# Kernel optimization log

Measured on AMD Instinct MI355X. Metric: run time of the kernel, lower is better.

The kernel has to match this reference:

```python
import jax, jax.numpy as jnp
import numpy as np

B, N, D, H = 4096, 64, 32, 64

def setup_inputs() -> dict:
    key = jax.random.key(0)
    ks = jax.random.split(key, 10)
    s = lambda fan_in: 1.0 / np.sqrt(fan_in)
    return {
        "joint_features": jax.random.normal(ks[0], (B, N, D), jnp.float32),
        "Wm1": jax.random.uniform(ks[1], (2 * D, H), jnp.float32, -s(2 * D), s(2 * D)),
        "bm1": jax.random.uniform(ks[2], (H,), jnp.float32, -s(2 * D), s(2 * D)),
        "Wm2": jax.random.uniform(ks[3], (H, D), jnp.float32, -s(H), s(H)),
        "bm2": jax.random.uniform(ks[4], (D,), jnp.float32, -s(H), s(H)),
        "Wu1": jax.random.uniform(ks[5], (2 * D, H), jnp.float32, -s(2 * D), s(2 * D)),
        "bu1": jax.random.uniform(ks[6], (H,), jnp.float32, -s(2 * D), s(2 * D)),
        "Wu2": jax.random.uniform(ks[7], (H, D), jnp.float32, -s(H), s(H)),
        "bu2": jax.random.uniform(ks[8], (D,), jnp.float32, -s(H), s(H)),
        "residual_weight": jnp.float32(0.5),
        "num_joints": N,
    }

def reference(joint_features, Wm1, bm1, Wm2, bm2, Wu1, bu1, Wu2, bu2, residual_weight, num_joints):
    n = num_joints
    # chain topology: directed edges (i->i+1) and (i+1->i); dst receives message
    dst = jnp.concatenate([jnp.arange(n - 1), jnp.arange(1, n)])  # [E]
    src = jnp.concatenate([jnp.arange(1, n), jnp.arange(n - 1)])  # [E]
    # edge gather + concat: [B, E, 2D]
    edge_in = jnp.concatenate([joint_features[:, dst], joint_features[:, src]], axis=-1)
    # message MLP (ReLU after both layers, per original Sequential)
    msg = jax.nn.relu(jax.nn.relu(edge_in @ Wm1 + bm1) @ Wm2 + bm2)  # [B, E, D]
    # scatter-add messages to destination nodes
    messages = jnp.zeros_like(joint_features).at[:, dst].add(msg)  # [B, N, D]
    # per-node update MLP on concat(feature, message)
    upd_in = jnp.concatenate([joint_features, messages], axis=-1)  # [B, N, 2D]
    updated = jax.nn.relu(upd_in @ Wu1 + bu1) @ Wu2 + bu2  # [B, N, D]
    return residual_weight * updated + (1.0 - residual_weight) * joint_features
```

## Files before the change

### kernel.cpp

```cpp
#include <hip/hip_runtime.h>
#include <hip/hip_bf16.h>


typedef __bf16 bf16x8 __attribute__((ext_vector_type(8)));
typedef float  f32x4  __attribute__((ext_vector_type(4)));
typedef unsigned short u16;

#define NBATCH 8
#define NBI 2
#define ITERS (NBATCH / NBI)
#define HS  72
#define MBS 40

__device__ __forceinline__ u16 f2b(float f) { return __builtin_bit_cast(u16, (__bf16)f); }
__device__ __forceinline__ f32x4 MFMA(bf16x8 a, bf16x8 b, f32x4 c) {
    return __builtin_amdgcn_mfma_f32_16x16x32_bf16(a, b, c, 0, 0, 0);
}
__device__ __forceinline__ bf16x8 pack8(float4 a, float4 b) {
    bf16x8 r = {(__bf16)a.x, (__bf16)a.y, (__bf16)a.z, (__bf16)a.w,
                (__bf16)b.x, (__bf16)b.y, (__bf16)b.z, (__bf16)b.w};
    return r;
}

__global__ __launch_bounds__(256, 2)
void agn_mfma(const float* __restrict__ x, const float* __restrict__ Wm1,
              const float* __restrict__ bm1, const float* __restrict__ Wm2,
              const float* __restrict__ bm2, const float* __restrict__ Wu1,
              const float* __restrict__ bu1, const float* __restrict__ Wu2,
              const float* __restrict__ bu2, const float* __restrict__ rw_p,
              float* __restrict__ out)
{
    __shared__ __align__(16) u16 sH[256 * HS];
    __shared__ __align__(16) u16 sMB[256 * MBS];

    const int t = threadIdx.x;
    const int w = t >> 6;
    const int lane = t & 63;
    const int ln = lane & 15;
    const int q  = lane >> 4;

    bf16x8 B1a[4], B1b[4], B2[2][2], B3[2][4], B4[2][2];
#pragma unroll
    for (int nt = 0; nt < 4; ++nt)
#pragma unroll
        for (int j = 0; j < 8; ++j) {
            B1a[nt][j] = (__bf16)Wm1[(q * 8 + j) * 64 + nt * 16 + ln];
            B1b[nt][j] = (__bf16)Wm1[(32 + q * 8 + j) * 64 + nt * 16 + ln];
        }
#pragma unroll
    for (int s = 0; s < 2; ++s)
#pragma unroll
        for (int nt = 0; nt < 2; ++nt)
#pragma unroll
            for (int j = 0; j < 8; ++j)
                B2[s][nt][j] = (__bf16)Wm2[(s * 32 + q * 8 + j) * 32 + nt * 16 + ln];
#pragma unroll
    for (int s = 0; s < 2; ++s)
#pragma unroll
        for (int nt = 0; nt < 4; ++nt)
#pragma unroll
            for (int j = 0; j < 8; ++j)
                B3[s][nt][j] = (__bf16)Wu1[(s * 32 + q * 8 + j) * 64 + nt * 16 + ln];
#pragma unroll
    for (int s = 0; s < 2; ++s)
#pragma unroll
        for (int nt = 0; nt < 2; ++nt)
#pragma unroll
            for (int j = 0; j < 8; ++j)
                B4[s][nt][j] = (__bf16)Wu2[(s * 32 + q * 8 + j) * 32 + nt * 16 + ln];

    float bm1v[4], bu1v[4], bm2v[2], bu2v[2];
#pragma unroll
    for (int nt = 0; nt < 4; ++nt) { bm1v[nt] = bm1[nt * 16 + ln]; bu1v[nt] = bu1[nt * 16 + ln]; }
#pragma unroll
    for (int nt = 0; nt < 2; ++nt) { bm2v[nt] = bm2[nt * 16 + ln]; bu2v[nt] = bu2[nt * 16 + ln]; }
    const float rw = rw_p[0];
    const float om = 1.f - rw;

    const size_t base = (size_t)blockIdx.x * (NBATCH * 64 * 32);

    for (int it = 0; it < ITERS; ++it) {
        const float* xit = x + base + (size_t)it * (NBI * 64 * 32);
        float*       oit = out + base + (size_t)it * (NBI * 64 * 32);

        {
            float4 xd[4][2], xsv[4][2];
#pragma unroll
            for (int m = 0; m < 4; ++m) {
                const int mt = 4 * w + m;
                const int erow = mt * 16 + ln;
                const int bb = erow >> 7;
                int e = erow & 127;
                if (e >= 126) e = 0;
                const int dst  = (e < 63) ? e : e - 62;
                const int srcn = (e < 63) ? e + 1 : e - 63;
                const float* pd = xit + ((bb << 6) + dst) * 32 + q * 8;
                const float* ps = xit + ((bb << 6) + srcn) * 32 + q * 8;
                xd[m][0] = *(const float4*)pd;  xd[m][1] = *(const float4*)(pd + 4);
                xsv[m][0] = *(const float4*)ps; xsv[m][1] = *(const float4*)(ps + 4);
            }
#pragma unroll
            for (int m = 0; m < 4; ++m) {
                const int mt = 4 * w + m;
                bf16x8 Ad = pack8(xd[m][0], xd[m][1]);
                bf16x8 As = pack8(xsv[m][0], xsv[m][1]);
#pragma unroll
                for (int nt = 0; nt < 4; ++nt) {
                    f32x4 acc = {0.f, 0.f, 0.f, 0.f};
                    acc = MFMA(Ad, B1a[nt], acc);
                    acc = MFMA(As, B1b[nt], acc);
                    const int rb = mt * 16 + q * 4;
                    const int c  = nt * 16 + ln;
#pragma unroll
                    for (int r = 0; r < 4; ++r)
                        sH[(rb + r) * HS + c] = f2b(fmaxf(acc[r] + bm1v[nt], 0.f));
                }
            }
        }
        __syncthreads();

#pragma unroll
        for (int m = 0; m < 4; ++m) {
            const int mt = 4 * w + m;
            const int row = mt * 16 + ln;
            bf16x8 A0 = __builtin_bit_cast(bf16x8, *(const uint4*)&sH[row * HS + q * 8]);
            bf16x8 A1 = __builtin_bit_cast(bf16x8, *(const uint4*)&sH[row * HS + 32 + q * 8]);
#pragma unroll
            for (int nt = 0; nt < 2; ++nt) {
                f32x4 acc = {0.f, 0.f, 0.f, 0.f};
                acc = MFMA(A0, B2[0][nt], acc);
                acc = MFMA(A1, B2[1][nt], acc);
                const int rb = mt * 16 + q * 4;
                const int c  = nt * 16 + ln;
#pragma unroll
                for (int r = 0; r < 4; ++r)
                    sMB[(rb + r) * MBS + c] = f2b(fmaxf(acc[r] + bm2v[nt], 0.f));
            }
        }
        __syncthreads();

#pragma unroll
        for (int m = 0; m < 2; ++m) {
            const int mt = 2 * w + m;
            const int row = mt * 16 + ln;
            const int bb = row >> 6;
            const int i2 = row & 63;
            const float* p = xit + row * 32 + q * 8;
            float4 a0 = *(const float4*)p;
            float4 a1 = *(const float4*)(p + 4);
            bf16x8 A0 = pack8(a0, a1);
            float mv[8] = {0.f, 0.f, 0.f, 0.f, 0.f, 0.f, 0.f, 0.f};
            if (i2 < 63) {
                uint4 u = *(const uint4*)&sMB[((bb << 7) + i2) * MBS + q * 8];
                const unsigned* pu = (const unsigned*)&u;
#pragma unroll
                for (int h = 0; h < 4; ++h) {
                    mv[2 * h]     += __uint_as_float(pu[h] << 16);
                    mv[2 * h + 1] += __uint_as_float(pu[h] & 0xFFFF0000u);
                }
            }
            if (i2 > 0) {
                uint4 u = *(const uint4*)&sMB[((bb << 7) + 62 + i2) * MBS + q * 8];
                const unsigned* pu = (const unsigned*)&u;
#pragma unroll
                for (int h = 0; h < 4; ++h) {
                    mv[2 * h]     += __uint_as_float(pu[h] << 16);
                    mv[2 * h + 1] += __uint_as_float(pu[h] & 0xFFFF0000u);
                }
            }
            bf16x8 A1;
#pragma unroll
            for (int j = 0; j < 8; ++j) A1[j] = (__bf16)mv[j];
#pragma unroll
            for (int nt = 0; nt < 4; ++nt) {
                f32x4 acc = {0.f, 0.f, 0.f, 0.f};
                acc = MFMA(A0, B3[0][nt], acc);
                acc = MFMA(A1, B3[1][nt], acc);
                const int rb = mt * 16 + q * 4;
                const int c  = nt * 16 + ln;
#pragma unroll
                for (int r = 0; r < 4; ++r)
                    sH[(rb + r) * HS + c] = f2b(fmaxf(acc[r] + bu1v[nt], 0.f));
            }
        }
        __syncthreads();

#pragma unroll
        for (int m = 0; m < 2; ++m) {
            const int mt = 2 * w + m;
            const int arow = mt * 16 + ln;
            bf16x8 A0 = __builtin_bit_cast(bf16x8, *(const uint4*)&sH[arow * HS + q * 8]);
            bf16x8 A1 = __builtin_bit_cast(bf16x8, *(const uint4*)&sH[arow * HS + 32 + q * 8]);
#pragma unroll
            for (int nt = 0; nt < 2; ++nt) {
                f32x4 acc = {0.f, 0.f, 0.f, 0.f};
                acc = MFMA(A0, B4[0][nt], acc);
                acc = MFMA(A1, B4[1][nt], acc);
                const int rb = mt * 16 + q * 4;
                const int c  = nt * 16 + ln;
#pragma unroll
                for (int r = 0; r < 4; ++r) {
                    const int off = (rb + r) * 32 + c;
                    oit[off] = rw * (acc[r] + bu2v[nt]) + om * xit[off];
                }
            }
        }
        __syncthreads();
    }
}

extern "C" void kernel_launch(void* const* d_in, const int* in_sizes, int n_in,
                              void* d_out, int out_size, void* d_ws, size_t ws_size,
                              hipStream_t stream) {
    const float* x   = (const float*)d_in[0];
    const float* Wm1 = (const float*)d_in[1];
    const float* bm1 = (const float*)d_in[2];
    const float* Wm2 = (const float*)d_in[3];
    const float* bm2 = (const float*)d_in[4];
    const float* Wu1 = (const float*)d_in[5];
    const float* bu1 = (const float*)d_in[6];
    const float* Wu2 = (const float*)d_in[7];
    const float* bu2 = (const float*)d_in[8];
    const float* rw  = (const float*)d_in[9];
    float* out = (float*)d_out;

    const int B = in_sizes[0] / (64 * 32);
    agn_mfma<<<B / NBATCH, 256, 0, stream>>>(x, Wm1, bm1, Wm2, bm2, Wu1, bu1, Wu2, bu2, rw, out);
}
```

Before: 121.7 us.

## Pre-pack bf16 weight fragments in prep kernel and launch one block per batch

Adds a small prep kernel that converts the weights into bf16 MFMA fragment layout in workspace, along with biases and the residual weight. The main kernel then loads each fragment with a single 16-byte read instead of many scalar converted loads. The main kernel now handles one batch element per block (4096 blocks) with half the LDS and occupancy hint 4, replacing 512 blocks that each looped over 8 batches. Weight fragments are loaded per phase to reduce register pressure, at the cost of an extra kernel launch and re-reading weights in every block.

```diff
diff --git a/kernel.cpp b/kernel.cpp
--- a/kernel.cpp
+++ b/kernel.cpp
@@ -6,9 +6,6 @@
 typedef float  f32x4  __attribute__((ext_vector_type(4)));
 typedef unsigned short u16;
 
-#define NBATCH 8
-#define NBI 2
-#define ITERS (NBATCH / NBI)
 #define HS  72
 #define MBS 40
 
@@ -22,16 +19,47 @@
     return r;
 }
 
-__global__ __launch_bounds__(256, 2)
-void agn_mfma(const float* __restrict__ x, const float* __restrict__ Wm1,
-              const float* __restrict__ bm1, const float* __restrict__ Wm2,
-              const float* __restrict__ bm2, const float* __restrict__ Wu1,
-              const float* __restrict__ bu1, const float* __restrict__ Wu2,
-              const float* __restrict__ bu2, const float* __restrict__ rw_p,
-              float* __restrict__ out)
+__global__ void agn_prep(const float* __restrict__ Wm1, const float* __restrict__ bm1,
+                         const float* __restrict__ Wm2, const float* __restrict__ bm2,
+                         const float* __restrict__ Wu1, const float* __restrict__ bu1,
+                         const float* __restrict__ Wu2, const float* __restrict__ bu2,
+                         const float* __restrict__ rw,
+                         u16* __restrict__ wsf, float* __restrict__ wsb)
 {
-    __shared__ __align__(16) u16 sH[256 * HS];
-    __shared__ __align__(16) u16 sMB[256 * MBS];
+    const int idx = blockIdx.x * 256 + threadIdx.x;
+    {
+        const int f = idx >> 9, r = idx & 511;
+        const int lane = r >> 3, j = r & 7;
+        const int ln = lane & 15, q = lane >> 4;
+        float v;
+        if (f < 4)       v = Wm1[(q * 8 + j) * 64 + f * 16 + ln];
+        else if (f < 8)  v = Wm1[(32 + q * 8 + j) * 64 + (f - 4) * 16 + ln];
+        else if (f < 12) { int s = (f - 8) >> 1, nt = (f - 8) & 1;  v = Wm2[(s * 32 + q * 8 + j) * 32 + nt * 16 + ln]; }
+        else if (f < 20) { int s = (f - 12) >> 2, nt = (f - 12) & 3; v = Wu1[(s * 32 + q * 8 + j) * 64 + nt * 16 + ln]; }
+        else             { int s = (f - 20) >> 1, nt = (f - 20) & 1; v = Wu2[(s * 32 + q * 8 + j) * 32 + nt * 16 + ln]; }
+        wsf[idx] = f2b(v);
+    }
+    if (blockIdx.x == 0) {
+        const int t = threadIdx.x;
+        if (t < 192) {
+            const int g = t >> 4, i = t & 15;
+            float v;
+            if (g < 4)       v = bm1[g * 16 + i];
+            else if (g < 6)  v = bm2[(g - 4) * 16 + i];
+            else if (g < 10) v = bu1[(g - 6) * 16 + i];
+            else             v = bu2[(g - 10) * 16 + i];
+            wsb[t] = v;
+        }
+        if (t == 255) wsb[192] = rw[0];
+    }
+}
+
+__global__ __launch_bounds__(256, 4)
+void agn_main(const float* __restrict__ x, const u16* __restrict__ wsf,
+              const float* __restrict__ wsb, float* __restrict__ out)
+{
+    __shared__ __align__(16) u16 sH[128 * HS];
+    __shared__ __align__(16) u16 sMB[128 * MBS];
 
     const int t = threadIdx.x;
     const int w = t >> 6;
@@ -39,89 +67,58 @@
     const int ln = lane & 15;
     const int q  = lane >> 4;
 
-    bf16x8 B1a[4], B1b[4], B2[2][2], B3[2][4], B4[2][2];
-#pragma unroll
-    for (int nt = 0; nt < 4; ++nt)
-#pragma unroll
-        for (int j = 0; j < 8; ++j) {
-            B1a[nt][j] = (__bf16)Wm1[(q * 8 + j) * 64 + nt * 16 + ln];
-            B1b[nt][j] = (__bf16)Wm1[(32 + q * 8 + j) * 64 + nt * 16 + ln];
-        }
-#pragma unroll
-    for (int s = 0; s < 2; ++s)
-#pragma unroll
-        for (int nt = 0; nt < 2; ++nt)
-#pragma unroll
-            for (int j = 0; j < 8; ++j)
-                B2[s][nt][j] = (__bf16)Wm2[(s * 32 + q * 8 + j) * 32 + nt * 16 + ln];
-#pragma unroll
-    for (int s = 0; s < 2; ++s)
-#pragma unroll
-        for (int nt = 0; nt < 4; ++nt)
-#pragma unroll
-            for (int j = 0; j < 8; ++j)
-                B3[s][nt][j] = (__bf16)Wu1[(s * 32 + q * 8 + j) * 64 + nt * 16 + ln];
-#pragma unroll
-    for (int s = 0; s < 2; ++s)
-#pragma unroll
-        for (int nt = 0; nt < 2; ++nt)
-#pragma unroll
-            for (int j = 0; j < 8; ++j)
-                B4[s][nt][j] = (__bf16)Wu2[(s * 32 + q * 8 + j) * 32 + nt * 16 + ln];
-
-    float bm1v[4], bu1v[4], bm2v[2], bu2v[2];
-#pragma unroll
-    for (int nt = 0; nt < 4; ++nt) { bm1v[nt] = bm1[nt * 16 + ln]; bu1v[nt] = bu1[nt * 16 + ln]; }
-#pragma unroll
-    for (int nt = 0; nt < 2; ++nt) { bm2v[nt] = bm2[nt * 16 + ln]; bu2v[nt] = bu2[nt * 16 + ln]; }
-    const float rw = rw_p[0];
-    const float om = 1.f - rw;
-
-    const size_t base = (size_t)blockIdx.x * (NBATCH * 64 * 32);
-
-    for (int it = 0; it < ITERS; ++it) {
-        const float* xit = x + base + (size_t)it * (NBI * 64 * 32);
-        float*       oit = out + base + (size_t)it * (NBI * 64 * 32);
-
-        {
-            float4 xd[4][2], xsv[4][2];
-#pragma unroll
-            for (int m = 0; m < 4; ++m) {
-                const int mt = 4 * w + m;
-                const int erow = mt * 16 + ln;
-                const int bb = erow >> 7;
-                int e = erow & 127;
-                if (e >= 126) e = 0;
-                const int dst  = (e < 63) ? e : e - 62;
-                const int srcn = (e < 63) ? e + 1 : e - 63;
-                const float* pd = xit + ((bb << 6) + dst) * 32 + q * 8;
-                const float* ps = xit + ((bb << 6) + srcn) * 32 + q * 8;
-                xd[m][0] = *(const float4*)pd;  xd[m][1] = *(const float4*)(pd + 4);
-                xsv[m][0] = *(const float4*)ps; xsv[m][1] = *(const float4*)(ps + 4);
-            }
-#pragma unroll
-            for (int m = 0; m < 4; ++m) {
-                const int mt = 4 * w + m;
-                bf16x8 Ad = pack8(xd[m][0], xd[m][1]);
-                bf16x8 As = pack8(xsv[m][0], xsv[m][1]);
-#pragma unroll
-                for (int nt = 0; nt < 4; ++nt) {
-                    f32x4 acc = {0.f, 0.f, 0.f, 0.f};
-                    acc = MFMA(Ad, B1a[nt], acc);
-                    acc = MFMA(As, B1b[nt], acc);
-                    const int rb = mt * 16 + q * 4;
-                    const int c  = nt * 16 + ln;
-#pragma unroll
-                    for (int r = 0; r < 4; ++r)
-                        sH[(rb + r) * HS + c] = f2b(fmaxf(acc[r] + bm1v[nt], 0.f));
-                }
-            }
-        }
-        __syncthreads();
-
-#pragma unroll
-        for (int m = 0; m < 4; ++m) {
-            const int mt = 4 * w + m;
+    const size_t base = (size_t)blockIdx.x * (64 * 32);
+    const float* xb = x + base;
+    float*       ob = out + base;
+
+    const u16* wf = wsf + lane * 8;
+#define LDFRAG(f) __builtin_bit_cast(bf16x8, *(const uint4*)(wf + ((f) << 9)))
+
+    {
+        bf16x8 B1a[4], B1b[4];
+#pragma unroll
+        for (int nt = 0; nt < 4; ++nt) { B1a[nt] = LDFRAG(nt); B1b[nt] = LDFRAG(4 + nt); }
+        float bm1v[4];
+#pragma unroll
+        for (int nt = 0; nt < 4; ++nt) bm1v[nt] = wsb[nt * 16 + ln];
+#pragma unroll
+        for (int m = 0; m < 2; ++m) {
+            const int mt = 2 * w + m;
+            int e = mt * 16 + ln;
+            if (e >= 126) e = 0;
+            const int dst  = (e < 63) ? e : e - 62;
+            const int srcn = (e < 63) ? e + 1 : e - 63;
+            const float* pd = xb + dst * 32 + q * 8;
+            const float* ps = xb + srcn * 32 + q * 8;
+            float4 d0 = *(const float4*)pd, d1 = *(const float4*)(pd + 4);
+            float4 s0 = *(const float4*)ps, s1 = *(const float4*)(ps + 4);
+            bf16x8 Ad = pack8(d0, d1);
+            bf16x8 As = pack8(s0, s1);
+#pragma unroll
+            for (int nt = 0; nt < 4; ++nt) {
+                f32x4 acc = {0.f, 0.f, 0.f, 0.f};
+                acc = MFMA(Ad, B1a[nt], acc);
+                acc = MFMA(As, B1b[nt], acc);
+                const int rb = mt * 16 + q * 4;
+                const int c  = nt * 16 + ln;
+#pragma unroll
+                for (int r = 0; r < 4; ++r)
+                    sH[(rb + r) * HS + c] = f2b(fmaxf(acc[r] + bm1v[nt], 0.f));
+            }
+        }
+    }
+    __syncthreads();
+
+    {
+        bf16x8 B2[2][2];
+#pragma unroll
+        for (int s = 0; s < 2; ++s)
+#pragma unroll
+            for (int nt = 0; nt < 2; ++nt) B2[s][nt] = LDFRAG(8 + s * 2 + nt);
+        float bm2v[2] = { wsb[64 + ln], wsb[80 + ln] };
+#pragma unroll
+        for (int m = 0; m < 2; ++m) {
+            const int mt = 2 * w + m;
             const int row = mt * 16 + ln;
             bf16x8 A0 = __builtin_bit_cast(bf16x8, *(const uint4*)&sH[row * HS + q * 8]);
             bf16x8 A1 = __builtin_bit_cast(bf16x8, *(const uint4*)&sH[row * HS + 32 + q * 8]);
@@ -137,76 +134,85 @@
                     sMB[(rb + r) * MBS + c] = f2b(fmaxf(acc[r] + bm2v[nt], 0.f));
             }
         }
-        __syncthreads();
-
-#pragma unroll
-        for (int m = 0; m < 2; ++m) {
-            const int mt = 2 * w + m;
-            const int row = mt * 16 + ln;
-            const int bb = row >> 6;
-            const int i2 = row & 63;
-            const float* p = xit + row * 32 + q * 8;
-            float4 a0 = *(const float4*)p;
-            float4 a1 = *(const float4*)(p + 4);
-            bf16x8 A0 = pack8(a0, a1);
-            float mv[8] = {0.f, 0.f, 0.f, 0.f, 0.f, 0.f, 0.f, 0.f};
-            if (i2 < 63) {
-                uint4 u = *(const uint4*)&sMB[((bb << 7) + i2) * MBS + q * 8];
-                const unsigned* pu = (const unsigned*)&u;
-#pragma unroll
-                for (int h = 0; h < 4; ++h) {
-                    mv[2 * h]     += __uint_as_float(pu[h] << 16);
-                    mv[2 * h + 1] += __uint_as_float(pu[h] & 0xFFFF0000u);
-                }
-            }
-            if (i2 > 0) {
-                uint4 u = *(const uint4*)&sMB[((bb << 7) + 62 + i2) * MBS + q * 8];
-                const unsigned* pu = (const unsigned*)&u;
-#pragma unroll
-                for (int h = 0; h < 4; ++h) {
-                    mv[2 * h]     += __uint_as_float(pu[h] << 16);
-                    mv[2 * h + 1] += __uint_as_float(pu[h] & 0xFFFF0000u);
-                }
-            }
-            bf16x8 A1;
-#pragma unroll
-            for (int j = 0; j < 8; ++j) A1[j] = (__bf16)mv[j];
-#pragma unroll
-            for (int nt = 0; nt < 4; ++nt) {
-                f32x4 acc = {0.f, 0.f, 0.f, 0.f};
-                acc = MFMA(A0, B3[0][nt], acc);
-                acc = MFMA(A1, B3[1][nt], acc);
-                const int rb = mt * 16 + q * 4;
-                const int c  = nt * 16 + ln;
-#pragma unroll
-                for (int r = 0; r < 4; ++r)
-                    sH[(rb + r) * HS + c] = f2b(fmaxf(acc[r] + bu1v[nt], 0.f));
-            }
-        }
-        __syncthreads();
-
-#pragma unroll
-        for (int m = 0; m < 2; ++m) {
-            const int mt = 2 * w + m;
-            const int arow = mt * 16 + ln;
-            bf16x8 A0 = __builtin_bit_cast(bf16x8, *(const uint4*)&sH[arow * HS + q * 8]);
-            bf16x8 A1 = __builtin_bit_cast(bf16x8, *(const uint4*)&sH[arow * HS + 32 + q * 8]);
-#pragma unroll
-            for (int nt = 0; nt < 2; ++nt) {
-                f32x4 acc = {0.f, 0.f, 0.f, 0.f};
-                acc = MFMA(A0, B4[0][nt], acc);
-                acc = MFMA(A1, B4[1][nt], acc);
-                const int rb = mt * 16 + q * 4;
-                const int c  = nt * 16 + ln;
-#pragma unroll
-                for (int r = 0; r < 4; ++r) {
-                    const int off = (rb + r) * 32 + c;
-                    oit[off] = rw * (acc[r] + bu2v[nt]) + om * xit[off];
-                }
-            }
-        }
-        __syncthreads();
-    }
+    }
+    __syncthreads();
+
+    {
+        bf16x8 B3[2][4];
+#pragma unroll
+        for (int s = 0; s < 2; ++s)
+#pragma unroll
+            for (int nt = 0; nt < 4; ++nt) B3[s][nt] = LDFRAG(12 + s * 4 + nt);
+        float bu1v[4];
+#pragma unroll
+        for (int nt = 0; nt < 4; ++nt) bu1v[nt] = wsb[96 + nt * 16 + ln];
+        const int row = w * 16 + ln;
+        const float* p = xb + row * 32 + q * 8;
+        float4 a0 = *(const float4*)p, a1 = *(const float4*)(p + 4);
+        bf16x8 A0 = pack8(a0, a1);
+        float mv[8] = {0.f, 0.f, 0.f, 0.f, 0.f, 0.f, 0.f, 0.f};
+        if (row < 63) {
+            uint4 u = *(const uint4*)&sMB[row * MBS + q * 8];
+            const unsigned* pu = (const unsigned*)&u;
+#pragma unroll
+            for (int h = 0; h < 4; ++h) {
+                mv[2 * h]     += __uint_as_float(pu[h] << 16);
+                mv[2 * h + 1] += __uint_as_float(pu[h] & 0xFFFF0000u);
+            }
+        }
+        if (row > 0) {
+            uint4 u = *(const uint4*)&sMB[(62 + row) * MBS + q * 8];
+            const unsigned* pu = (const unsigned*)&u;
+#pragma unroll
+            for (int h = 0; h < 4; ++h) {
+                mv[2 * h]     += __uint_as_float(pu[h] << 16);
+                mv[2 * h + 1] += __uint_as_float(pu[h] & 0xFFFF0000u);
+            }
+        }
+        bf16x8 A1;
+#pragma unroll
+        for (int j = 0; j < 8; ++j) A1[j] = (__bf16)mv[j];
+#pragma unroll
+        for (int nt = 0; nt < 4; ++nt) {
+            f32x4 acc = {0.f, 0.f, 0.f, 0.f};
+            acc = MFMA(A0, B3[0][nt], acc);
+            acc = MFMA(A1, B3[1][nt], acc);
+            const int rb = w * 16 + q * 4;
+            const int c  = nt * 16 + ln;
+#pragma unroll
+            for (int r = 0; r < 4; ++r)
+                sH[(rb + r) * HS + c] = f2b(fmaxf(acc[r] + bu1v[nt], 0.f));
+        }
+    }
+    __syncthreads();
+
+    {
+        bf16x8 B4[2][2];
+#pragma unroll
+        for (int s = 0; s < 2; ++s)
+#pragma unroll
+            for (int nt = 0; nt < 2; ++nt) B4[s][nt] = LDFRAG(20 + s * 2 + nt);
+        float bu2v[2] = { wsb[160 + ln], wsb[176 + ln] };
+        const float rw = wsb[192];
+        const float om = 1.f - rw;
+        const int arow = w * 16 + ln;
+        bf16x8 A0 = __builtin_bit_cast(bf16x8, *(const uint4*)&sH[arow * HS + q * 8]);
+        bf16x8 A1 = __builtin_bit_cast(bf16x8, *(const uint4*)&sH[arow * HS + 32 + q * 8]);
+#pragma unroll
+        for (int nt = 0; nt < 2; ++nt) {
+            f32x4 acc = {0.f, 0.f, 0.f, 0.f};
+            acc = MFMA(A0, B4[0][nt], acc);
+            acc = MFMA(A1, B4[1][nt], acc);
+            const int rb = w * 16 + q * 4;
+            const int c  = nt * 16 + ln;
+#pragma unroll
+            for (int r = 0; r < 4; ++r) {
+                const int off = (rb + r) * 32 + c;
+                ob[off] = rw * (acc[r] + bu2v[nt]) + om * xb[off];
+            }
+        }
+    }
+#undef LDFRAG
 }
 
 extern "C" void kernel_launch(void* const* d_in, const int* in_sizes, int n_in,
@@ -224,6 +230,10 @@
     const float* rw  = (const float*)d_in[9];
     float* out = (float*)d_out;
 
+    u16*   wsf = (u16*)d_ws;
+    float* wsb = (float*)((char*)d_ws + 24576);
+
     const int B = in_sizes[0] / (64 * 32);
-    agn_mfma<<<B / NBATCH, 256, 0, stream>>>(x, Wm1, bm1, Wm2, bm2, Wu1, bu1, Wu2, bu2, rw, out);
-}
+    agn_prep<<<48, 256, 0, stream>>>(Wm1, bm1, Wm2, bm2, Wu1, bu1, Wu2, bu2, rw, wsf, wsb);
+    agn_main<<<B, 256, 0, stream>>>(x, wsf, wsb, out);
+}
```

After: 127.2 us. 1.05x slower.
